# Kernel optimization log

Hardware: AMD Instinct MI355X
Metric: run time of the kernel (lower is better)

The kernel has to match this reference:

```python
import jax, jax.numpy as jnp
import numpy as np

VOL = 64          # self.vol_size
SPACE = 0.2       # space_size (cubic), space_center = 0
IMG = 255.0       # normalization constant in the source (2*u/255 - 1)


def setup_inputs() -> dict:
    key = jax.random.key(0)
    ks = jax.random.split(key, 5)
    B, V, C, Hf, Wf = 2, 4, 32, 64, 64
    features = jax.random.normal(ks[0], (B, V, C, Hf, Wf), jnp.float32)
    # near-identity rotations, cameras ~0.5m away, focal ~200, principal point 128
    camera_R = jnp.eye(3, dtype=jnp.float32)[None, None] + 0.01 * jax.random.normal(ks[1], (B, V, 3, 3), jnp.float32)
    camera_T = jnp.array([0.0, 0.0, 0.5], jnp.float32) + 0.01 * jax.random.normal(ks[2], (B, V, 3), jnp.float32)
    K0 = jnp.array([[200.0, 0.0, 128.0], [0.0, 200.0, 128.0], [0.0, 0.0, 1.0]], jnp.float32)
    Kmask = jnp.array([[1.0, 0.0, 1.0], [0.0, 1.0, 1.0], [0.0, 0.0, 0.0]], jnp.float32)
    camera_K = K0[None, None] + 0.5 * jax.random.normal(ks[3], (B, V, 3, 3), jnp.float32) * Kmask
    root_world = 0.01 * jax.random.normal(ks[4], (B, 3), jnp.float32)
    return dict(features=features, camera_R=camera_R, camera_T=camera_T,
                camera_K=camera_K, root_world=root_world)


def _bilinear_sample(feat, x, y):
    """PyTorch F.grid_sample, mode=bilinear, padding=zeros, align_corners=False.
    feat: [N,C,H,W]; x,y: [N,P] pixel-space coords (already unnormalized).
    Returns [N,C,P]."""
    N, C, H, W = feat.shape
    x0 = jnp.floor(x); y0 = jnp.floor(y)
    x1 = x0 + 1.0;     y1 = y0 + 1.0
    wx1 = x - x0; wx0 = 1.0 - wx1
    wy1 = y - y0; wy0 = 1.0 - wy1
    feat_flat = feat.reshape(N, C, H * W)

    def gather(xi, yi, w):
        valid = (xi >= 0) & (xi <= W - 1) & (yi >= 0) & (yi <= H - 1)
        xi_c = jnp.clip(xi, 0, W - 1).astype(jnp.int32)
        yi_c = jnp.clip(yi, 0, H - 1).astype(jnp.int32)
        idx = yi_c * W + xi_c                                   # [N,P]
        vals = jnp.take_along_axis(feat_flat, idx[:, None, :], axis=2)  # [N,C,P]
        return vals * (w * valid.astype(feat.dtype))[:, None, :]

    return (gather(x0, y0, wx0 * wy0) + gather(x1, y0, wx1 * wy0)
            + gather(x0, y1, wx0 * wy1) + gather(x1, y1, wx1 * wy1))


def reference(features, camera_R, camera_T, camera_K, root_world):
    B, V, C, Hf, Wf = features.shape
    D = VOL
    # _build_grid: 64^3 points, xyz order, spanning SPACE around center 0
    r = jnp.arange(D, dtype=jnp.float32)
    z, y, x = jnp.meshgrid(r, r, r, indexing='ij')
    grid = jnp.stack([x, y, z], axis=0) / (D - 1)               # [3,D,D,D]
    pts = ((grid - 0.5) * SPACE).reshape(3, -1).T               # [P,3], P = D^3
    # relative camera translation: new_T = R @ root + T
    new_T = jnp.einsum('bvij,bj->bvi', camera_R, root_world) + camera_T
    # project: pts_cam = pts @ R^T + T  -> [B,V,P,3]
    pts_cam = jnp.einsum('pj,bvij->bvpi', pts, camera_R) + new_T[:, :, None, :]
    zc = jnp.maximum(pts_cam[..., 2], 1e-5)
    fx = camera_K[:, :, 0, 0][..., None]; fy = camera_K[:, :, 1, 1][..., None]
    cx = camera_K[:, :, 0, 2][..., None]; cy = camera_K[:, :, 1, 2][..., None]
    u = pts_cam[..., 0] * fx / zc + cx
    v = pts_cam[..., 1] * fy / zc + cy
    u_n = 2.0 * u / IMG - 1.0
    v_n = 2.0 * v / IMG - 1.0
    # unnormalize (align_corners=False): ix = ((g+1)*W - 1)/2
    px = ((u_n + 1.0) * Wf - 1.0) * 0.5
    py = ((v_n + 1.0) * Hf - 1.0) * 0.5
    feat_bv = features.reshape(B * V, C, Hf, Wf)
    vol = _bilinear_sample(feat_bv, px.reshape(B * V, -1), py.reshape(B * V, -1))  # [BV,C,P]
    vol = vol.reshape(B, V, C, D, D, D).mean(axis=1)            # average over views
    return vol
```

## Files before the change

kernel.cpp:

```cpp
#include <hip/hip_runtime.h>

#define B_   2
#define V_   4
#define C_   32
#define HW_  4096
#define D_   64
#define P_   (D_*D_*D_)
#define SCL_ (64.0f/255.0f)

typedef _Float16 half2v __attribute__((ext_vector_type(2)));

union Corner16 { uint4 u; half2v h[4]; };

__global__ __launch_bounds__(256) void tx_kernel(const float* __restrict__ in,
                                                 unsigned int* __restrict__ out) {
    __shared__ float tile[32][65];
    const int bv  = blockIdx.x >> 6;
    const int hw0 = (blockIdx.x & 63) << 6;
    const int t   = threadIdx.x;
    const float* src = in + (size_t)bv * C_ * HW_ + hw0;
#pragma unroll
    for (int i = 0; i < 8; ++i) {
        int e = t + (i << 8);
        tile[e >> 6][e & 63] = src[(e >> 6) * HW_ + (e & 63)];
    }
    __syncthreads();
    unsigned int* dst = out + ((size_t)bv * HW_ + hw0) * (C_ / 2);
#pragma unroll
    for (int i = 0; i < 4; ++i) {
        int idx = t + (i << 8);
        int c  = (idx << 1) & 31;
        int hw = idx >> 4;
        half2v v = { (_Float16)tile[c][hw], (_Float16)tile[c + 1][hw] };
        dst[idx] = *(unsigned int*)&v;
    }
}

__global__ __launch_bounds__(256) void vol_kernel(
    const unsigned char* __restrict__ feat,
    const float* __restrict__ Rm,
    const float* __restrict__ Tm,
    const float* __restrict__ Km,
    const float* __restrict__ root,
    float* __restrict__ out)
{
    __shared__ __align__(16) float cam[4][20];

    const int t = threadIdx.x;
    const int q = t & 3;
    const int b = blockIdx.x >> 12;
    const int p = ((blockIdx.x & 4095) << 6) | (t >> 2);

    if (t < 4) {
        const int bv = b * V_ + t;
        const float* Rb = Rm + bv * 9;
        const float* Tb = Tm + bv * 3;
        const float* Kb = Km + bv * 9;
        const float rx = root[b*3+0], ry = root[b*3+1], rz = root[b*3+2];
        cam[t][0] = Rb[0]; cam[t][1] = Rb[1]; cam[t][2] = Rb[2];
        cam[t][3] = Rb[0]*rx + Rb[1]*ry + Rb[2]*rz + Tb[0];
        cam[t][4] = Rb[3]; cam[t][5] = Rb[4]; cam[t][6] = Rb[5];
        cam[t][7] = Rb[3]*rx + Rb[4]*ry + Rb[5]*rz + Tb[1];
        cam[t][8] = Rb[6]; cam[t][9] = Rb[7]; cam[t][10] = Rb[8];
        cam[t][11] = Rb[6]*rx + Rb[7]*ry + Rb[8]*rz + Tb[2];
        cam[t][12] = Kb[0] * SCL_;
        cam[t][13] = Kb[4] * SCL_;
        cam[t][14] = Kb[2] * SCL_ - 0.5f;
        cam[t][15] = Kb[5] * SCL_ - 0.5f;
    }
    __syncthreads();

    const int xi = p & 63, yi = (p >> 6) & 63, zi = p >> 12;
    const float X = ((float)xi * (1.0f/63.0f) - 0.5f) * 0.2f;
    const float Y = ((float)yi * (1.0f/63.0f) - 0.5f) * 0.2f;
    const float Z = ((float)zi * (1.0f/63.0f) - 0.5f) * 0.2f;

    const float4 cA = *(const float4*)&cam[q][0];
    const float4 cB = *(const float4*)&cam[q][4];
    const float4 cC = *(const float4*)&cam[q][8];
    const float4 cK = *(const float4*)&cam[q][12];
    const float xc = cA.x*X + cA.y*Y + cA.z*Z + cA.w;
    const float yc = cB.x*X + cB.y*Y + cB.z*Z + cB.w;
    float zc       = cC.x*X + cC.y*Y + cC.z*Z + cC.w;
    zc = fmaxf(zc, 1e-5f);
    const float inv = 1.0f / zc;
    const float px = (xc * inv) * cK.x + cK.z;
    const float py = (yc * inv) * cK.y + cK.w;

    const float x0f = floorf(px), y0f = floorf(py);
    const float wx1 = px - x0f, wx0 = 1.0f - wx1;
    const float wy1 = py - y0f, wy0 = 1.0f - wy1;
    const float x1f = x0f + 1.0f, y1f = y0f + 1.0f;
    const float vx0 = (x0f >= 0.0f && x0f <= 63.0f) ? 1.0f : 0.0f;
    const float vx1 = (x1f >= 0.0f && x1f <= 63.0f) ? 1.0f : 0.0f;
    const float vy0 = (y0f >= 0.0f && y0f <= 63.0f) ? 1.0f : 0.0f;
    const float vy1 = (y1f >= 0.0f && y1f <= 63.0f) ? 1.0f : 0.0f;
    const float w00 = wx0*wy0*vx0*vy0*0.25f, w01 = wx1*wy0*vx1*vy0*0.25f;
    const float w10 = wx0*wy1*vx0*vy1*0.25f, w11 = wx1*wy1*vx1*vy1*0.25f;
    const int x0c = (int)fminf(fmaxf(x0f, 0.0f), 63.0f);
    const int x1c = (int)fminf(fmaxf(x1f, 0.0f), 63.0f);
    const int y0c = (int)fminf(fmaxf(y0f, 0.0f), 63.0f);
    const int y1c = (int)fminf(fmaxf(y1f, 0.0f), 63.0f);
    const int bvbase = (b * V_ + q) * HW_;
    const int o00 = (bvbase + y0c*64 + x0c) << 6;
    const int o01 = (bvbase + y0c*64 + x1c) << 6;
    const int o10 = (bvbase + y1c*64 + x0c) << 6;
    const int o11 = (bvbase + y1c*64 + x1c) << 6;

    float acc[8];
#pragma unroll
    for (int j = 0; j < 8; ++j) acc[j] = 0.0f;

    const unsigned char* fb = feat + (q << 4);
    const int lane_base = t & ~3;

#pragma unroll
    for (int v = 0; v < V_; ++v) {
        const int src = lane_base | v;
        const float sw00 = __shfl(w00, src), sw01 = __shfl(w01, src);
        const float sw10 = __shfl(w10, src), sw11 = __shfl(w11, src);
        const int so00 = __shfl(o00, src), so01 = __shfl(o01, src);
        const int so10 = __shfl(o10, src), so11 = __shfl(o11, src);

        const Corner16 c00 = *(const Corner16*)(fb + (size_t)(unsigned)so00);
        const Corner16 c01 = *(const Corner16*)(fb + (size_t)(unsigned)so01);
        const Corner16 c10 = *(const Corner16*)(fb + (size_t)(unsigned)so10);
        const Corner16 c11 = *(const Corner16*)(fb + (size_t)(unsigned)so11);

        const half2v h00 = { (_Float16)sw00, (_Float16)sw00 };
        const half2v h01 = { (_Float16)sw01, (_Float16)sw01 };
        const half2v h10 = { (_Float16)sw10, (_Float16)sw10 };
        const half2v h11 = { (_Float16)sw11, (_Float16)sw11 };
#pragma unroll
        for (int j = 0; j < 4; ++j) {
            half2v s = c00.h[j] * h00;
            s += c01.h[j] * h01;
            s += c10.h[j] * h10;
            s += c11.h[j] * h11;
            acc[2*j+0] += (float)s.x;
            acc[2*j+1] += (float)s.y;
        }
    }

    float* ob = out + ((size_t)(b * C_) + (q << 3)) * P_ + p;
#pragma unroll
    for (int j = 0; j < 8; ++j)
        __builtin_nontemporal_store(acc[j], ob + (size_t)j * P_);
}

__global__ __launch_bounds__(256) void vol_fallback(
    const float* __restrict__ feat,
    const float* __restrict__ Rm, const float* __restrict__ Tm,
    const float* __restrict__ Km, const float* __restrict__ root,
    float* __restrict__ out)
{
    const int b = blockIdx.x >> 10;
    const int p = ((blockIdx.x & 1023) << 8) | threadIdx.x;
    const int xi = p & 63, yi = (p >> 6) & 63, zi = p >> 12;
    const float X = ((float)xi * (1.0f/63.0f) - 0.5f) * 0.2f;
    const float Y = ((float)yi * (1.0f/63.0f) - 0.5f) * 0.2f;
    const float Z = ((float)zi * (1.0f/63.0f) - 0.5f) * 0.2f;
    float acc[C_];
#pragma unroll
    for (int c = 0; c < C_; ++c) acc[c] = 0.0f;
    const float rx = root[b*3+0], ry = root[b*3+1], rz = root[b*3+2];
#pragma unroll
    for (int v = 0; v < V_; ++v) {
        const int bv = b * V_ + v;
        const float* Rb = Rm + bv * 9; const float* Tb = Tm + bv * 3;
        const float* Kb = Km + bv * 9;
        const float r00=Rb[0], r01=Rb[1], r02=Rb[2];
        const float r10=Rb[3], r11=Rb[4], r12=Rb[5];
        const float r20=Rb[6], r21=Rb[7], r22=Rb[8];
        const float t0 = r00*rx + r01*ry + r02*rz + Tb[0];
        const float t1 = r10*rx + r11*ry + r12*rz + Tb[1];
        const float t2 = r20*rx + r21*ry + r22*rz + Tb[2];
        const float xc = r00*X + r01*Y + r02*Z + t0;
        const float yc = r10*X + r11*Y + r12*Z + t1;
        float zc       = r20*X + r21*Y + r22*Z + t2;
        zc = fmaxf(zc, 1e-5f);
        const float inv = 1.0f / zc;
        const float px = xc * (Kb[0]*SCL_) * inv + (Kb[2]*SCL_ - 0.5f);
        const float py = yc * (Kb[4]*SCL_) * inv + (Kb[5]*SCL_ - 0.5f);
        const float x0f = floorf(px), y0f = floorf(py);
        const float wx1 = px - x0f, wx0 = 1.0f - wx1;
        const float wy1 = py - y0f, wy0 = 1.0f - wy1;
        const float x1f = x0f + 1.0f, y1f = y0f + 1.0f;
        const float vx0 = (x0f >= 0.0f && x0f <= 63.0f) ? 1.0f : 0.0f;
        const float vx1 = (x1f >= 0.0f && x1f <= 63.0f) ? 1.0f : 0.0f;
        const float vy0 = (y0f >= 0.0f && y0f <= 63.0f) ? 1.0f : 0.0f;
        const float vy1 = (y1f >= 0.0f && y1f <= 63.0f) ? 1.0f : 0.0f;
        const float w00 = wx0*wy0*vx0*vy0, w01 = wx1*wy0*vx1*vy0;
        const float w10 = wx0*wy1*vx0*vy1, w11 = wx1*wy1*vx1*vy1;
        const int x0c = (int)fminf(fmaxf(x0f, 0.0f), 63.0f);
        const int x1c = (int)fminf(fmaxf(x1f, 0.0f), 63.0f);
        const int y0c = (int)fminf(fmaxf(y0f, 0.0f), 63.0f);
        const int y1c = (int)fminf(fmaxf(y1f, 0.0f), 63.0f);
        const float* fb = feat + (size_t)bv * C_ * HW_;
        const int i00 = y0c*64 + x0c, i01 = y0c*64 + x1c;
        const int i10 = y1c*64 + x0c, i11 = y1c*64 + x1c;
#pragma unroll
        for (int c = 0; c < C_; ++c) {
            const float* f = fb + c * HW_;
            acc[c] += w00*f[i00] + w01*f[i01] + w10*f[i10] + w11*f[i11];
        }
    }
    float* ob = out + (size_t)b * C_ * P_ + p;
#pragma unroll
    for (int c = 0; c < C_; ++c) ob[(size_t)c * P_] = acc[c] * 0.25f;
}

extern "C" void kernel_launch(void* const* d_in, const int* in_sizes, int n_in,
                              void* d_out, int out_size, void* d_ws, size_t ws_size,
                              hipStream_t stream) {
    const float* feat = (const float*)d_in[0];
    const float* Rm   = (const float*)d_in[1];
    const float* Tm   = (const float*)d_in[2];
    const float* Km   = (const float*)d_in[3];
    const float* root = (const float*)d_in[4];
    float* out = (float*)d_out;

    const size_t need = (size_t)B_ * V_ * HW_ * C_ * sizeof(_Float16);
    if (ws_size >= need) {
        unsigned int* ftx = (unsigned int*)d_ws;
        tx_kernel<<<B_ * V_ * 64, 256, 0, stream>>>(feat, ftx);
        vol_kernel<<<B_ * P_ / 64, 256, 0, stream>>>(
            (const unsigned char*)ftx, Rm, Tm, Km, root, out);
    } else {
        vol_fallback<<<B_ * P_ / 256, 256, 0, stream>>>(feat, Rm, Tm, Km, root, out);
    }
}
```

Before: 102.0 us.

## Split each voxel across two lanes with 16 channels each and fp16 accumulation

Each voxel now goes to two lanes instead of four. Each lane projects two views and trades results with its partner through a single xor-shuffle, which replaces the eight indexed shuffles per view. Each lane gathers 32-byte corners covering 16 channels and keeps the accumulation across views in packed fp16, with weights converted by cvt_pkrtz. The goal is to cut shuffle and conversion overhead and to use wider loads, at the cost of higher register pressure and lower precision from accumulating in fp16.

```diff
diff --git a/kernel.cpp b/kernel.cpp
--- a/kernel.cpp
+++ b/kernel.cpp
@@ -9,8 +9,10 @@
 #define SCL_ (64.0f/255.0f)
 
 typedef _Float16 half2v __attribute__((ext_vector_type(2)));
-
-union Corner16 { uint4 u; half2v h[4]; };
+typedef __fp16  fp16x2 __attribute__((ext_vector_type(2)));
+
+union Corner32 { uint4 u[2]; half2v h[8]; };
+union H2U { half2v h; fp16x2 f; unsigned int u; };
 
 __global__ __launch_bounds__(256) void tx_kernel(const float* __restrict__ in,
                                                  unsigned int* __restrict__ out) {
@@ -47,9 +49,9 @@
     __shared__ __align__(16) float cam[4][20];
 
     const int t = threadIdx.x;
-    const int q = t & 3;
-    const int b = blockIdx.x >> 12;
-    const int p = ((blockIdx.x & 4095) << 6) | (t >> 2);
+    const int h = t & 1;
+    const int b = blockIdx.x >> 11;
+    const int p = ((blockIdx.x & 2047) << 7) | (t >> 1);
 
     if (t < 4) {
         const int bv = b * V_ + t;
@@ -75,77 +77,91 @@
     const float Y = ((float)yi * (1.0f/63.0f) - 0.5f) * 0.2f;
     const float Z = ((float)zi * (1.0f/63.0f) - 0.5f) * 0.2f;
 
-    const float4 cA = *(const float4*)&cam[q][0];
-    const float4 cB = *(const float4*)&cam[q][4];
-    const float4 cC = *(const float4*)&cam[q][8];
-    const float4 cK = *(const float4*)&cam[q][12];
-    const float xc = cA.x*X + cA.y*Y + cA.z*Z + cA.w;
-    const float yc = cB.x*X + cB.y*Y + cB.z*Z + cB.w;
-    float zc       = cC.x*X + cC.y*Y + cC.z*Z + cC.w;
-    zc = fmaxf(zc, 1e-5f);
-    const float inv = 1.0f / zc;
-    const float px = (xc * inv) * cK.x + cK.z;
-    const float py = (yc * inv) * cK.y + cK.w;
-
-    const float x0f = floorf(px), y0f = floorf(py);
-    const float wx1 = px - x0f, wx0 = 1.0f - wx1;
-    const float wy1 = py - y0f, wy0 = 1.0f - wy1;
-    const float x1f = x0f + 1.0f, y1f = y0f + 1.0f;
-    const float vx0 = (x0f >= 0.0f && x0f <= 63.0f) ? 1.0f : 0.0f;
-    const float vx1 = (x1f >= 0.0f && x1f <= 63.0f) ? 1.0f : 0.0f;
-    const float vy0 = (y0f >= 0.0f && y0f <= 63.0f) ? 1.0f : 0.0f;
-    const float vy1 = (y1f >= 0.0f && y1f <= 63.0f) ? 1.0f : 0.0f;
-    const float w00 = wx0*wy0*vx0*vy0*0.25f, w01 = wx1*wy0*vx1*vy0*0.25f;
-    const float w10 = wx0*wy1*vx0*vy1*0.25f, w11 = wx1*wy1*vx1*vy1*0.25f;
-    const int x0c = (int)fminf(fmaxf(x0f, 0.0f), 63.0f);
-    const int x1c = (int)fminf(fmaxf(x1f, 0.0f), 63.0f);
-    const int y0c = (int)fminf(fmaxf(y0f, 0.0f), 63.0f);
-    const int y1c = (int)fminf(fmaxf(y1f, 0.0f), 63.0f);
-    const int bvbase = (b * V_ + q) * HW_;
-    const int o00 = (bvbase + y0c*64 + x0c) << 6;
-    const int o01 = (bvbase + y0c*64 + x1c) << 6;
-    const int o10 = (bvbase + y1c*64 + x0c) << 6;
-    const int o11 = (bvbase + y1c*64 + x1c) << 6;
-
-    float acc[8];
-#pragma unroll
-    for (int j = 0; j < 8; ++j) acc[j] = 0.0f;
-
-    const unsigned char* fb = feat + (q << 4);
-    const int lane_base = t & ~3;
-
-#pragma unroll
-    for (int v = 0; v < V_; ++v) {
-        const int src = lane_base | v;
-        const float sw00 = __shfl(w00, src), sw01 = __shfl(w01, src);
-        const float sw10 = __shfl(w10, src), sw11 = __shfl(w11, src);
-        const int so00 = __shfl(o00, src), so01 = __shfl(o01, src);
-        const int so10 = __shfl(o10, src), so11 = __shfl(o11, src);
-
-        const Corner16 c00 = *(const Corner16*)(fb + (size_t)(unsigned)so00);
-        const Corner16 c01 = *(const Corner16*)(fb + (size_t)(unsigned)so01);
-        const Corner16 c10 = *(const Corner16*)(fb + (size_t)(unsigned)so10);
-        const Corner16 c11 = *(const Corner16*)(fb + (size_t)(unsigned)so11);
-
-        const half2v h00 = { (_Float16)sw00, (_Float16)sw00 };
-        const half2v h01 = { (_Float16)sw01, (_Float16)sw01 };
-        const half2v h10 = { (_Float16)sw10, (_Float16)sw10 };
-        const half2v h11 = { (_Float16)sw11, (_Float16)sw11 };
-#pragma unroll
-        for (int j = 0; j < 4; ++j) {
-            half2v s = c00.h[j] * h00;
-            s += c01.h[j] * h01;
-            s += c10.h[j] * h10;
-            s += c11.h[j] * h11;
-            acc[2*j+0] += (float)s.x;
-            acc[2*j+1] += (float)s.y;
+    unsigned int Wp[4][4];
+    int          Op[4][4];
+
+#pragma unroll
+    for (int i = 0; i < 2; ++i) {
+        const int v = (h << 1) | i;
+        const float4 cA = *(const float4*)&cam[v][0];
+        const float4 cB = *(const float4*)&cam[v][4];
+        const float4 cC = *(const float4*)&cam[v][8];
+        const float4 cK = *(const float4*)&cam[v][12];
+        const float xc = cA.x*X + cA.y*Y + cA.z*Z + cA.w;
+        const float yc = cB.x*X + cB.y*Y + cB.z*Z + cB.w;
+        float zc       = cC.x*X + cC.y*Y + cC.z*Z + cC.w;
+        zc = fmaxf(zc, 1e-5f);
+        const float inv = 1.0f / zc;
+        const float px = (xc * inv) * cK.x + cK.z;
+        const float py = (yc * inv) * cK.y + cK.w;
+
+        const float x0f = floorf(px), y0f = floorf(py);
+        const float wx1 = px - x0f, wx0 = 1.0f - wx1;
+        const float wy1 = py - y0f, wy0 = 1.0f - wy1;
+        const float x1f = x0f + 1.0f, y1f = y0f + 1.0f;
+        const float vx0 = (x0f >= 0.0f && x0f <= 63.0f) ? 0.25f : 0.0f;
+        const float vx1 = (x1f >= 0.0f && x1f <= 63.0f) ? 0.25f : 0.0f;
+        const float vy0 = (y0f >= 0.0f && y0f <= 63.0f) ? 1.0f : 0.0f;
+        const float vy1 = (y1f >= 0.0f && y1f <= 63.0f) ? 1.0f : 0.0f;
+        const float w00 = wx0*wy0*vx0*vy0, w01 = wx1*wy0*vx1*vy0;
+        const float w10 = wx0*wy1*vx0*vy1, w11 = wx1*wy1*vx1*vy1;
+        H2U u0, u1, u2, u3;
+        u0.f = __builtin_amdgcn_cvt_pkrtz(w00, w00); Wp[i][0] = u0.u;
+        u1.f = __builtin_amdgcn_cvt_pkrtz(w01, w01); Wp[i][1] = u1.u;
+        u2.f = __builtin_amdgcn_cvt_pkrtz(w10, w10); Wp[i][2] = u2.u;
+        u3.f = __builtin_amdgcn_cvt_pkrtz(w11, w11); Wp[i][3] = u3.u;
+
+        const int x0c = (int)fminf(fmaxf(x0f, 0.0f), 63.0f);
+        const int x1c = (int)fminf(fmaxf(x1f, 0.0f), 63.0f);
+        const int y0c = (int)fminf(fmaxf(y0f, 0.0f), 63.0f);
+        const int y1c = (int)fminf(fmaxf(y1f, 0.0f), 63.0f);
+        const int bvbase = (b * V_ + v) * HW_;
+        Op[i][0] = (bvbase + y0c*64 + x0c) << 6;
+        Op[i][1] = (bvbase + y0c*64 + x1c) << 6;
+        Op[i][2] = (bvbase + y1c*64 + x0c) << 6;
+        Op[i][3] = (bvbase + y1c*64 + x1c) << 6;
+    }
+
+#pragma unroll
+    for (int i = 0; i < 2; ++i) {
+#pragma unroll
+        for (int k = 0; k < 4; ++k) {
+            Wp[2+i][k] = (unsigned int)__shfl_xor((int)Wp[i][k], 1);
+            Op[2+i][k] = __shfl_xor(Op[i][k], 1);
         }
     }
 
-    float* ob = out + ((size_t)(b * C_) + (q << 3)) * P_ + p;
-#pragma unroll
-    for (int j = 0; j < 8; ++j)
-        __builtin_nontemporal_store(acc[j], ob + (size_t)j * P_);
+    const half2v z2 = { (_Float16)0.0f, (_Float16)0.0f };
+    half2v acc[8];
+#pragma unroll
+    for (int j = 0; j < 8; ++j) acc[j] = z2;
+
+    const unsigned char* base = feat + (h << 5);
+#pragma unroll
+    for (int s = 0; s < 4; ++s) {
+        const Corner32 c00 = *(const Corner32*)(base + (size_t)(unsigned)Op[s][0]);
+        const Corner32 c01 = *(const Corner32*)(base + (size_t)(unsigned)Op[s][1]);
+        const Corner32 c10 = *(const Corner32*)(base + (size_t)(unsigned)Op[s][2]);
+        const Corner32 c11 = *(const Corner32*)(base + (size_t)(unsigned)Op[s][3]);
+        H2U w0; w0.u = Wp[s][0];
+        H2U w1; w1.u = Wp[s][1];
+        H2U w2; w2.u = Wp[s][2];
+        H2U w3; w3.u = Wp[s][3];
+#pragma unroll
+        for (int j = 0; j < 8; ++j) {
+            acc[j] += c00.h[j] * w0.h;
+            acc[j] += c01.h[j] * w1.h;
+            acc[j] += c10.h[j] * w2.h;
+            acc[j] += c11.h[j] * w3.h;
+        }
+    }
+
+    float* ob = out + ((size_t)(b * C_) + (h << 4)) * P_ + p;
+#pragma unroll
+    for (int j = 0; j < 8; ++j) {
+        __builtin_nontemporal_store((float)acc[j].x, ob + (size_t)(2*j  ) * P_);
+        __builtin_nontemporal_store((float)acc[j].y, ob + (size_t)(2*j+1) * P_);
+    }
 }
 
 __global__ __launch_bounds__(256) void vol_fallback(
@@ -224,7 +240,7 @@
     if (ws_size >= need) {
         unsigned int* ftx = (unsigned int*)d_ws;
         tx_kernel<<<B_ * V_ * 64, 256, 0, stream>>>(feat, ftx);
-        vol_kernel<<<B_ * P_ / 64, 256, 0, stream>>>(
+        vol_kernel<<<B_ * P_ / 128, 256, 0, stream>>>(
             (const unsigned char*)ftx, Rm, Tm, Km, root, out);
     } else {
         vol_fallback<<<B_ * P_ / 256, 256, 0, stream>>>(feat, Rm, Tm, Km, root, out);
```

Result: slower. 106.6 us (+4.5%).
